# Kernel tuning notes

Hardware: AMD Instinct MI355X
Metric: run time of the kernel (lower is better)

## Reference

```python
import jax, jax.numpy as jnp
import numpy as np

CODEBOOK_SIZE = 1024
LATENT_DIM = 64
BETA = 0.25

def setup_inputs() -> dict:
    key = jax.random.key(0)
    k1, k2 = jax.random.split(key)
    B, C, T = 32, LATENT_DIM, 4096
    x = jax.random.normal(k1, (B, C, T), dtype=jnp.float32)
    # codebook initialized uniform(-1/K, 1/K) as in the torch module
    emb = jax.random.uniform(k2, (CODEBOOK_SIZE, LATENT_DIM), dtype=jnp.float32,
                             minval=-1.0 / CODEBOOK_SIZE, maxval=1.0 / CODEBOOK_SIZE)
    return {"x": x, "emb": emb}

def reference(x, emb):
    B, C, T = x.shape  # C == LATENT_DIM
    xf = jnp.transpose(x, (0, 2, 1)).reshape(B * T, C)  # [BT, D]
    d = (jnp.sum(xf * xf, axis=-1, keepdims=True)
         + jnp.sum(emb * emb, axis=-1)[None, :]
         - 2.0 * jnp.matmul(xf, emb.T))  # [BT, K]
    idx = jnp.argmin(d, axis=-1)  # [BT] int
    q = emb[idx].reshape(B, T, C).transpose(0, 2, 1)  # [B, C, T]
    commitment_loss = BETA * jnp.mean((jax.lax.stop_gradient(q) - x) ** 2)
    codebook_loss = jnp.mean((q - jax.lax.stop_gradient(x)) ** 2)
    quant_out = x + jax.lax.stop_gradient(q - x)  # straight-through
    return quant_out, codebook_loss, commitment_loss, idx.reshape(B, T)
```

## Files before the change

### kernel.cpp

```cpp
#include <hip/hip_runtime.h>


typedef unsigned long long u64;
typedef unsigned short u16;
typedef __attribute__((ext_vector_type(8))) short bf8_t;
typedef __attribute__((ext_vector_type(4))) float f4_t;

#define KCB 1024
#define DD 64
#define BB 32
#define TT 4096
#define BT (BB * TT)
#define NELEM (BB * DD * TT)

#define RPB 128
#define NT 16
#define FB_MAX 48
#define BAND 4e-5f

#define WS_LOSS 0
#define WS_E2 64
#define WS_EH 2048
#define WS_EL 34816

static __device__ __forceinline__ u16 bf16rte(float f) {
    unsigned u = __float_as_uint(f);
    return (u16)((u + 0x7FFFu + ((u >> 16) & 1u)) >> 16);
}
static __device__ __forceinline__ unsigned flipf(float f) {
    unsigned u = __float_as_uint(f);
    return (u & 0x80000000u) ? ~u : (u | 0x80000000u);
}
static __device__ __forceinline__ int fragidx(int n, int d) {
    return 1024 * (n >> 4) + 512 * (d >> 5) + 128 * ((d >> 3) & 3)
         + 8 * (n & 15) + (d & 7);
}

__global__ void vq_prep(const float* __restrict__ emb, float* __restrict__ ws) {
#pragma clang fp contract(off)
    const int tid = threadIdx.x;
    const int kl = tid >> 6, d = tid & 63;
    const int k = blockIdx.x * 4 + kl;
    if (blockIdx.x == 0 && tid == 0) ws[WS_LOSS] = 0.0f;
    __shared__ float sq[4][64];
    __shared__ float rsh[4][8];
    float v = emb[(size_t)k * DD + d];
    u16 hb = bf16rte(v);
    float hv = __uint_as_float((unsigned)hb << 16);
    u16 lb = bf16rte(v - hv);
    u16* ehg = (u16*)(ws + WS_EH) + 4096 * (k >> 6);
    u16* elg = (u16*)(ws + WS_EL) + 4096 * (k >> 6);
    const int ia = fragidx(k & 63, d);
    ehg[ia] = hb; elg[ia] = lb;
    sq[kl][d] = v * v;
    __syncthreads();
    if (tid < 32) {
        const int g = tid >> 3, j = tid & 7;
        float r = sq[g][j];
#pragma unroll
        for (int i = 1; i < 8; ++i) r += sq[g][8 * i + j];
        rsh[g][j] = r;
    }
    __syncthreads();
    if (tid < 4) {
        const float* r = rsh[tid];
        ws[WS_E2 + blockIdx.x * 4 + tid] =
            ((r[0] + r[1]) + (r[2] + r[3])) + ((r[4] + r[5]) + (r[6] + r[7]));
    }
}

__launch_bounds__(256, 4)
__global__ void vq_main(const float* __restrict__ x, const float* __restrict__ emb,
                        float* __restrict__ out, float* __restrict__ ws) {
#pragma clang fp contract(off)
    const int tid = threadIdx.x;
    const int lane = tid & 63;
    const int w = __builtin_amdgcn_readfirstlane(tid >> 6);
    const int l15 = lane & 15, q = lane >> 4;

    const int row0 = blockIdx.x * RPB;
    const int b = row0 >> 12;
    const int t0 = row0 & (TT - 1);

    __shared__ __align__(16) char arena[32768];
    u16* xhT = (u16*)arena;
    u16* xlT = (u16*)(arena + 16384);
    float* efs = (float*)arena;
    float* xfb = (float*)(arena + 16640);

    __shared__ float e2l[KCB];
    __shared__ float Srow[RPB];
    __shared__ int kwin[RPB];
    __shared__ int fbrows[FB_MAX];
    __shared__ int fbcnt;
    __shared__ float bsum;

    if (tid == 0) { fbcnt = 0; bsum = 0.0f; }
#pragma unroll
    for (int i = tid; i < KCB; i += 256) e2l[i] = ws[WS_E2 + i];

    if (tid < RPB) {
        const int r = tid;
        const float* xr = x + (size_t)b * DD * TT + t0 + r;
        const int gb = 1024 * (r >> 4);
        float rr[8];
#pragma unroll
        for (int i = 0; i < 64; i += 8) {
#pragma unroll
            for (int j = 0; j < 8; ++j) {
                float v = xr[(size_t)(i + j) * TT];
                if (i == 0) rr[j] = v * v; else rr[j] += v * v;
                u16 hb = bf16rte(v);
                float hv = __uint_as_float((unsigned)hb << 16);
                u16 lb = bf16rte(v - hv);
                const int ia = gb + fragidx(r & 15, i + j);
                xhT[ia] = hb; xlT[ia] = lb;
            }
        }
        Srow[r] = ((rr[0] + rr[1]) + (rr[2] + rr[3])) + ((rr[4] + rr[5]) + (rr[6] + rr[7]));
    }
    __syncthreads();

    bf8_t ah[2][2], al[2][2];
#pragma unroll
    for (int g = 0; g < 2; ++g) {
        const int gg = 2 * w + g;
        ah[g][0] = *(const bf8_t*)&xhT[1024 * gg + 8 * lane];
        ah[g][1] = *(const bf8_t*)&xhT[1024 * gg + 512 + 8 * lane];
        al[g][0] = *(const bf8_t*)&xlT[1024 * gg + 8 * lane];
        al[g][1] = *(const bf8_t*)&xlT[1024 * gg + 512 + 8 * lane];
    }
    float Sv[8];
#pragma unroll
    for (int g = 0; g < 2; ++g)
#pragma unroll
        for (int rg = 0; rg < 4; ++rg)
            Sv[4 * g + rg] = Srow[32 * w + 16 * g + 4 * q + rg];

    float v1[8], v2[8], kf[8];
#pragma unroll
    for (int s = 0; s < 8; ++s) { v1[s] = 3.4e38f; v2[s] = 3.4e38f; kf[s] = 0.0f; }

    const u16* ehg = (const u16*)(ws + WS_EH);
    const u16* elg = (const u16*)(ws + WS_EL);

    auto kstep = [&](float e2v, float kcol,
                     bf8_t bh0, bf8_t bl0, bf8_t bh1, bf8_t bl1) {
#pragma unroll
        for (int g = 0; g < 2; ++g) {
            f4_t acc = (f4_t){0.f, 0.f, 0.f, 0.f};
            acc = __builtin_amdgcn_mfma_f32_16x16x32_bf16(ah[g][0], bh0, acc, 0, 0, 0);
            acc = __builtin_amdgcn_mfma_f32_16x16x32_bf16(ah[g][0], bl0, acc, 0, 0, 0);
            acc = __builtin_amdgcn_mfma_f32_16x16x32_bf16(al[g][0], bh0, acc, 0, 0, 0);
            acc = __builtin_amdgcn_mfma_f32_16x16x32_bf16(ah[g][1], bh1, acc, 0, 0, 0);
            acc = __builtin_amdgcn_mfma_f32_16x16x32_bf16(ah[g][1], bl1, acc, 0, 0, 0);
            acc = __builtin_amdgcn_mfma_f32_16x16x32_bf16(al[g][1], bh1, acc, 0, 0, 0);
#pragma unroll
            for (int rg = 0; rg < 4; ++rg) {
                const int s = 4 * g + rg;
                float ck = Sv[s] + e2v;
                float u = __builtin_fmaf(-2.0f, acc[rg], ck);
                bool lt = u < v1[s];
                float sp = lt ? v1[s] : u;
                v2[s] = fminf(v2[s], sp);
                kf[s] = lt ? kcol : kf[s];
                v1[s] = fminf(v1[s], u);
            }
        }
    };

    bf8_t cbh0 = *(const bf8_t*)&ehg[8 * lane];
    bf8_t cbh1 = *(const bf8_t*)&ehg[512 + 8 * lane];
    bf8_t cbl0 = *(const bf8_t*)&elg[8 * lane];
    bf8_t cbl1 = *(const bf8_t*)&elg[512 + 8 * lane];
    float ce2 = e2l[l15];
#pragma unroll 2
    for (int it = 0; it < 63; ++it) {
        const u16* bhp = ehg + 1024 * (it + 1);
        const u16* blp = elg + 1024 * (it + 1);
        bf8_t nbh0 = *(const bf8_t*)&bhp[8 * lane];
        bf8_t nbh1 = *(const bf8_t*)&bhp[512 + 8 * lane];
        bf8_t nbl0 = *(const bf8_t*)&blp[8 * lane];
        bf8_t nbl1 = *(const bf8_t*)&blp[512 + 8 * lane];
        float ne2 = e2l[16 * (it + 1) + l15];
        kstep(ce2, (float)(16 * it + l15), cbh0, cbl0, cbh1, cbl1);
        cbh0 = nbh0; cbh1 = nbh1; cbl0 = nbl0; cbl1 = nbl1; ce2 = ne2;
    }
    kstep(ce2, (float)(16 * 63 + l15), cbh0, cbl0, cbh1, cbl1);

#pragma unroll
    for (int m = 1; m < 16; m <<= 1) {
#pragma unroll
        for (int s = 0; s < 8; ++s) {
            float ov1 = __shfl_xor(v1[s], m, 16);
            float okf = __shfl_xor(kf[s], m, 16);
            float ov2 = __shfl_xor(v2[s], m, 16);
            float nmx = fmaxf(v1[s], ov1);
            v2[s] = fminf(fminf(v2[s], ov2), nmx);
            bool lt = ov1 < v1[s];
            kf[s] = lt ? okf : kf[s];
            v1[s] = fminf(v1[s], ov1);
        }
    }
    if (l15 == 0) {
#pragma unroll
        for (int g = 0; g < 2; ++g)
#pragma unroll
            for (int rg = 0; rg < 4; ++rg) {
                const int s = 4 * g + rg;
                const int r = 32 * w + 16 * g + 4 * q + rg;
                kwin[r] = (int)kf[s];
                if (v2[s] <= v1[s] + BAND) {
                    int i = atomicAdd(&fbcnt, 1);
                    if (i < FB_MAX) fbrows[i] = r;
                }
            }
    }
    __syncthreads();

    const int cnt = min(fbcnt, FB_MAX);
    if (cnt > 0) {
        for (int i = tid; i < cnt * 64; i += 256) {
            int fi = i >> 6, l = i & 63;
            xfb[fi * 65 + l] = x[(size_t)b * DD * TT + (size_t)l * TT + t0 + fbrows[fi]];
        }
        u64 pmin[12];
#pragma unroll
        for (int sl = 0; sl < 12; ++sl) pmin[sl] = ~0ull;
#pragma unroll 1
        for (int T2 = 0; T2 < NT; ++T2) {
            __syncthreads();
            {
                const int n = tid >> 2, qd = (tid & 3) * 16;
                const float* sp = emb + (size_t)(T2 * 64 + n) * DD + qd;
                float* dp = efs + n * 65 + qd;
#pragma unroll
                for (int j = 0; j < 16; ++j) dp[j] = sp[j];
            }
            __syncthreads();
#pragma unroll
            for (int sl = 0; sl < 12; ++sl) {
                const int fi = w + 4 * sl;
                if (fi < cnt) {
                    float acc = 0.0f;
#pragma unroll
                    for (int i = 0; i < 64; ++i)
                        acc = __builtin_fmaf(efs[lane * 65 + i], xfb[fi * 65 + i], acc);
                    float ck = Srow[fbrows[fi]] + e2l[T2 * 64 + lane];
                    float u = __builtin_fmaf(-2.0f, acc, ck);
                    u64 pk = ((u64)flipf(u) << 10) | (unsigned)(T2 * 64 + lane);
                    pmin[sl] = pmin[sl] < pk ? pmin[sl] : pk;
                }
            }
        }
#pragma unroll
        for (int sl = 0; sl < 12; ++sl) {
            const int fi = w + 4 * sl;
            if (fi < cnt) {
                u64 pk = pmin[sl];
#pragma unroll
                for (int dl = 32; dl > 0; dl >>= 1) {
                    u64 o = __shfl_xor(pk, dl);
                    pk = o < pk ? o : pk;
                }
                if (lane == 0) kwin[fbrows[fi]] = (int)(pk & 1023u);
            }
        }
        __syncthreads();
    }

    if (tid < RPB) out[NELEM + 2 + row0 + tid] = (float)kwin[tid];

    const int r = tid & 127, c0 = (tid >> 7) * 32;
    const int kw = kwin[r];
    const float* eqr = emb + (size_t)kw * DD;
    float lsum = 0.0f;
#pragma unroll 8
    for (int i = 0; i < 32; ++i) {
        const int c = c0 + i;
        const size_t o = (size_t)b * DD * TT + (size_t)c * TT + t0 + r;
        float qv = eqr[c];
        float xv = x[o];
        out[o] = qv;
        float a = qv - xv;
        lsum = __builtin_fmaf(a, a, lsum);
    }
#pragma unroll
    for (int off = 32; off > 0; off >>= 1) lsum += __shfl_down(lsum, off);
    if (lane == 0) atomicAdd(&bsum, lsum);
    __syncthreads();
    if (tid == 0) atomicAdd(ws + WS_LOSS, bsum);
}

__global__ void vq_finalize(const float* __restrict__ ws, float* __restrict__ out) {
    if (threadIdx.x == 0 && blockIdx.x == 0) {
        float M = ws[WS_LOSS] / (float)NELEM;
        out[NELEM + 0] = M;
        out[NELEM + 1] = 0.25f * M;
    }
}

extern "C" void kernel_launch(void* const* d_in, const int* in_sizes, int n_in,
                              void* d_out, int out_size, void* d_ws, size_t ws_size,
                              hipStream_t stream) {
    const float* x = (const float*)d_in[0];
    const float* emb = (const float*)d_in[1];
    float* out = (float*)d_out;
    float* ws = (float*)d_ws;

    vq_prep<<<KCB / 4, 256, 0, stream>>>(emb, ws);
    vq_main<<<BT / RPB, 256, 0, stream>>>(x, emb, out, ws);
    vq_finalize<<<1, 64, 0, stream>>>(ws, out);
}
```

Measured before the change: 192.0 us.

## Split x staging across all threads, simplify fallback rescoring, fuse finalize via last-block counter

The x load and bf16 hi/lo split now uses all 256 threads, each doing half the channels, with partial squared norms combined through shared memory. The fallback exact-distance pass no longer stages codebook tiles and x rows in LDS behind per-tile barriers. Each warp instead handles its rows independently, reading emb from global and broadcasting x with shuffles. The separate finalize kernel is removed: the last block, found with an atomic counter, writes the loss, which saves a launch but adds fences and an atomic per block.

```diff
diff --git a/kernel.cpp b/kernel.cpp
--- a/kernel.cpp
+++ b/kernel.cpp
@@ -16,9 +16,11 @@
 #define RPB 128
 #define NT 16
 #define FB_MAX 48
+#define NSL 12
 #define BAND 4e-5f
 
 #define WS_LOSS 0
+#define WS_CNT 1
 #define WS_E2 64
 #define WS_EH 2048
 #define WS_EL 34816
@@ -41,7 +43,10 @@
     const int tid = threadIdx.x;
     const int kl = tid >> 6, d = tid & 63;
     const int k = blockIdx.x * 4 + kl;
-    if (blockIdx.x == 0 && tid == 0) ws[WS_LOSS] = 0.0f;
+    if (blockIdx.x == 0 && tid == 0) {
+        ws[WS_LOSS] = 0.0f;
+        ((unsigned*)ws)[WS_CNT] = 0u;
+    }
     __shared__ float sq[4][64];
     __shared__ float rsh[4][8];
     float v = emb[(size_t)k * DD + d];
@@ -85,11 +90,10 @@
     __shared__ __align__(16) char arena[32768];
     u16* xhT = (u16*)arena;
     u16* xlT = (u16*)(arena + 16384);
-    float* efs = (float*)arena;
-    float* xfb = (float*)(arena + 16640);
 
     __shared__ float e2l[KCB];
     __shared__ float Srow[RPB];
+    __shared__ float pbuf[RPB];
     __shared__ int kwin[RPB];
     __shared__ int fbrows[FB_MAX];
     __shared__ int fbcnt;
@@ -99,27 +103,31 @@
 #pragma unroll
     for (int i = tid; i < KCB; i += 256) e2l[i] = ws[WS_E2 + i];
 
-    if (tid < RPB) {
-        const int r = tid;
-        const float* xr = x + (size_t)b * DD * TT + t0 + r;
-        const int gb = 1024 * (r >> 4);
-        float rr[8];
+    const int r_ = tid & 127, h_ = tid >> 7;
+    float pp;
+    {
+        const float* xr = x + (size_t)b * DD * TT + t0 + r_;
+        const int gb = 1024 * (r_ >> 4);
+        float rr[4];
 #pragma unroll
         for (int i = 0; i < 64; i += 8) {
 #pragma unroll
-            for (int j = 0; j < 8; ++j) {
+            for (int jj = 0; jj < 4; ++jj) {
+                const int j = 4 * h_ + jj;
                 float v = xr[(size_t)(i + j) * TT];
-                if (i == 0) rr[j] = v * v; else rr[j] += v * v;
+                if (i == 0) rr[jj] = v * v; else rr[jj] += v * v;
                 u16 hb = bf16rte(v);
                 float hv = __uint_as_float((unsigned)hb << 16);
                 u16 lb = bf16rte(v - hv);
-                const int ia = gb + fragidx(r & 15, i + j);
+                const int ia = gb + fragidx(r_ & 15, i + j);
                 xhT[ia] = hb; xlT[ia] = lb;
             }
         }
-        Srow[r] = ((rr[0] + rr[1]) + (rr[2] + rr[3])) + ((rr[4] + rr[5]) + (rr[6] + rr[7]));
-    }
-    __syncthreads();
+        pp = (rr[0] + rr[1]) + (rr[2] + rr[3]);
+        if (h_ == 0) pbuf[r_] = pp;
+    }
+    __syncthreads();
+    if (h_ == 1) Srow[r_] = pbuf[r_] + pp;
 
     bf8_t ah[2][2], al[2][2];
 #pragma unroll
@@ -130,6 +138,7 @@
         al[g][0] = *(const bf8_t*)&xlT[1024 * gg + 8 * lane];
         al[g][1] = *(const bf8_t*)&xlT[1024 * gg + 512 + 8 * lane];
     }
+    __syncthreads();
     float Sv[8];
 #pragma unroll
     for (int g = 0; g < 2; ++g)
@@ -220,50 +229,32 @@
 
     const int cnt = min(fbcnt, FB_MAX);
     if (cnt > 0) {
-        for (int i = tid; i < cnt * 64; i += 256) {
-            int fi = i >> 6, l = i & 63;
-            xfb[fi * 65 + l] = x[(size_t)b * DD * TT + (size_t)l * TT + t0 + fbrows[fi]];
-        }
-        u64 pmin[12];
-#pragma unroll
-        for (int sl = 0; sl < 12; ++sl) pmin[sl] = ~0ull;
 #pragma unroll 1
-        for (int T2 = 0; T2 < NT; ++T2) {
-            __syncthreads();
-            {
-                const int n = tid >> 2, qd = (tid & 3) * 16;
-                const float* sp = emb + (size_t)(T2 * 64 + n) * DD + qd;
-                float* dp = efs + n * 65 + qd;
-#pragma unroll
-                for (int j = 0; j < 16; ++j) dp[j] = sp[j];
-            }
-            __syncthreads();
-#pragma unroll
-            for (int sl = 0; sl < 12; ++sl) {
-                const int fi = w + 4 * sl;
-                if (fi < cnt) {
+        for (int sl = 0; sl < NSL; ++sl) {
+            const int fi = w + 4 * sl;
+            if (fi < cnt) {
+                const int fr = fbrows[fi];
+                const float xv = x[(size_t)b * DD * TT + (size_t)lane * TT + t0 + fr];
+                const float srw = Srow[fr];
+                u64 pmin = ~0ull;
+#pragma unroll 1
+                for (int T2 = 0; T2 < NT; ++T2) {
+                    const float* er = emb + (size_t)(T2 * 64 + lane) * DD;
                     float acc = 0.0f;
 #pragma unroll
                     for (int i = 0; i < 64; ++i)
-                        acc = __builtin_fmaf(efs[lane * 65 + i], xfb[fi * 65 + i], acc);
-                    float ck = Srow[fbrows[fi]] + e2l[T2 * 64 + lane];
+                        acc = __builtin_fmaf(er[i], __shfl(xv, i), acc);
+                    float ck = srw + e2l[T2 * 64 + lane];
                     float u = __builtin_fmaf(-2.0f, acc, ck);
                     u64 pk = ((u64)flipf(u) << 10) | (unsigned)(T2 * 64 + lane);
-                    pmin[sl] = pmin[sl] < pk ? pmin[sl] : pk;
+                    pmin = pmin < pk ? pmin : pk;
                 }
-            }
-        }
-#pragma unroll
-        for (int sl = 0; sl < 12; ++sl) {
-            const int fi = w + 4 * sl;
-            if (fi < cnt) {
-                u64 pk = pmin[sl];
 #pragma unroll
                 for (int dl = 32; dl > 0; dl >>= 1) {
-                    u64 o = __shfl_xor(pk, dl);
-                    pk = o < pk ? o : pk;
+                    u64 o = __shfl_xor(pmin, dl);
+                    pmin = o < pmin ? o : pmin;
                 }
-                if (lane == 0) kwin[fbrows[fi]] = (int)(pk & 1023u);
+                if (lane == 0) kwin[fr] = (int)(pmin & 1023u);
             }
         }
         __syncthreads();
@@ -289,14 +280,17 @@
     for (int off = 32; off > 0; off >>= 1) lsum += __shfl_down(lsum, off);
     if (lane == 0) atomicAdd(&bsum, lsum);
     __syncthreads();
-    if (tid == 0) atomicAdd(ws + WS_LOSS, bsum);
-}
-
-__global__ void vq_finalize(const float* __restrict__ ws, float* __restrict__ out) {
-    if (threadIdx.x == 0 && blockIdx.x == 0) {
-        float M = ws[WS_LOSS] / (float)NELEM;
-        out[NELEM + 0] = M;
-        out[NELEM + 1] = 0.25f * M;
+
+    if (tid == 0) {
+        atomicAdd(ws + WS_LOSS, bsum);
+        __threadfence();
+        unsigned done = atomicAdd(&((unsigned*)ws)[WS_CNT], 1u);
+        if (done == (unsigned)(gridDim.x - 1)) {
+            __threadfence();
+            float M = atomicAdd(ws + WS_LOSS, 0.0f) / (float)NELEM;
+            out[NELEM + 0] = M;
+            out[NELEM + 1] = 0.25f * M;
+        }
     }
 }
 
@@ -310,5 +304,4 @@
 
     vq_prep<<<KCB / 4, 256, 0, stream>>>(emb, ws);
     vq_main<<<BT / RPB, 256, 0, stream>>>(x, emb, out, ws);
-    vq_finalize<<<1, 64, 0, stream>>>(ws, out);
-}
+}
```

New measurement: 280.9 us. 46.3% more time.

## Split codebook scan across two wave halves with 512-thread blocks and LDS merge

Applied to the files above, without the earlier changes.

Doubles the block to 512 threads. The two groups of four waves each scan half of the codebook for the same 128 rows, then merge their top-2 distances and argmins through shared memory before the fallback check. The fallback and output loops are rebalanced for the larger thread count. The aim is more waves in flight to hide MFMA and global-load latency, at the cost of extra barriers, a merge step, and possible occupancy limits from register pressure under launch_bounds(512,4).

```diff
diff --git a/kernel.cpp b/kernel.cpp
--- a/kernel.cpp
+++ b/kernel.cpp
@@ -14,8 +14,10 @@
 #define NELEM (BB * DD * TT)
 
 #define RPB 128
+#define NTHR 512
 #define NT 16
 #define FB_MAX 48
+#define NSL 6
 #define BAND 4e-5f
 
 #define WS_LOSS 0
@@ -69,13 +71,15 @@
     }
 }
 
-__launch_bounds__(256, 4)
+__launch_bounds__(NTHR, 4)
 __global__ void vq_main(const float* __restrict__ x, const float* __restrict__ emb,
                         float* __restrict__ out, float* __restrict__ ws) {
 #pragma clang fp contract(off)
     const int tid = threadIdx.x;
     const int lane = tid & 63;
     const int w = __builtin_amdgcn_readfirstlane(tid >> 6);
+    const int w4 = w & 3;
+    const int h = w >> 2;
     const int l15 = lane & 15, q = lane >> 4;
 
     const int row0 = blockIdx.x * RPB;
@@ -85,6 +89,9 @@
     __shared__ __align__(16) char arena[32768];
     u16* xhT = (u16*)arena;
     u16* xlT = (u16*)(arena + 16384);
+    float* mv1 = (float*)arena;
+    float* mv2 = (float*)(arena + 512);
+    float* mkf = (float*)(arena + 1024);
     float* efs = (float*)arena;
     float* xfb = (float*)(arena + 16640);
 
@@ -97,7 +104,7 @@
 
     if (tid == 0) { fbcnt = 0; bsum = 0.0f; }
 #pragma unroll
-    for (int i = tid; i < KCB; i += 256) e2l[i] = ws[WS_E2 + i];
+    for (int i = tid; i < KCB; i += NTHR) e2l[i] = ws[WS_E2 + i];
 
     if (tid < RPB) {
         const int r = tid;
@@ -124,7 +131,7 @@
     bf8_t ah[2][2], al[2][2];
 #pragma unroll
     for (int g = 0; g < 2; ++g) {
-        const int gg = 2 * w + g;
+        const int gg = 2 * w4 + g;
         ah[g][0] = *(const bf8_t*)&xhT[1024 * gg + 8 * lane];
         ah[g][1] = *(const bf8_t*)&xhT[1024 * gg + 512 + 8 * lane];
         al[g][0] = *(const bf8_t*)&xlT[1024 * gg + 8 * lane];
@@ -135,7 +142,8 @@
     for (int g = 0; g < 2; ++g)
 #pragma unroll
         for (int rg = 0; rg < 4; ++rg)
-            Sv[4 * g + rg] = Srow[32 * w + 16 * g + 4 * q + rg];
+            Sv[4 * g + rg] = Srow[32 * w4 + 16 * g + 4 * q + rg];
+    __syncthreads();
 
     float v1[8], v2[8], kf[8];
 #pragma unroll
@@ -169,13 +177,15 @@
         }
     };
 
-    bf8_t cbh0 = *(const bf8_t*)&ehg[8 * lane];
-    bf8_t cbh1 = *(const bf8_t*)&ehg[512 + 8 * lane];
-    bf8_t cbl0 = *(const bf8_t*)&elg[8 * lane];
-    bf8_t cbl1 = *(const bf8_t*)&elg[512 + 8 * lane];
-    float ce2 = e2l[l15];
+    const int it0 = 32 * h;
+    bf8_t cbh0 = *(const bf8_t*)&ehg[1024 * it0 + 8 * lane];
+    bf8_t cbh1 = *(const bf8_t*)&ehg[1024 * it0 + 512 + 8 * lane];
+    bf8_t cbl0 = *(const bf8_t*)&elg[1024 * it0 + 8 * lane];
+    bf8_t cbl1 = *(const bf8_t*)&elg[1024 * it0 + 512 + 8 * lane];
+    float ce2 = e2l[16 * it0 + l15];
 #pragma unroll 2
-    for (int it = 0; it < 63; ++it) {
+    for (int io = 0; io < 31; ++io) {
+        const int it = it0 + io;
         const u16* bhp = ehg + 1024 * (it + 1);
         const u16* blp = elg + 1024 * (it + 1);
         bf8_t nbh0 = *(const bf8_t*)&bhp[8 * lane];
@@ -186,7 +196,7 @@
         kstep(ce2, (float)(16 * it + l15), cbh0, cbl0, cbh1, cbl1);
         cbh0 = nbh0; cbh1 = nbh1; cbl0 = nbl0; cbl1 = nbl1; ce2 = ne2;
     }
-    kstep(ce2, (float)(16 * 63 + l15), cbh0, cbl0, cbh1, cbl1);
+    kstep(ce2, (float)(16 * (it0 + 31) + l15), cbh0, cbl0, cbh1, cbl1);
 
 #pragma unroll
     for (int m = 1; m < 16; m <<= 1) {
@@ -202,15 +212,33 @@
             v1[s] = fminf(v1[s], ov1);
         }
     }
-    if (l15 == 0) {
+
+    if (h == 1 && l15 == 0) {
 #pragma unroll
         for (int g = 0; g < 2; ++g)
 #pragma unroll
             for (int rg = 0; rg < 4; ++rg) {
                 const int s = 4 * g + rg;
-                const int r = 32 * w + 16 * g + 4 * q + rg;
-                kwin[r] = (int)kf[s];
-                if (v2[s] <= v1[s] + BAND) {
+                const int r = 32 * w4 + 16 * g + 4 * q + rg;
+                mv1[r] = v1[s]; mv2[r] = v2[s]; mkf[r] = kf[s];
+            }
+    }
+    __syncthreads();
+    if (h == 0 && l15 == 0) {
+#pragma unroll
+        for (int g = 0; g < 2; ++g)
+#pragma unroll
+            for (int rg = 0; rg < 4; ++rg) {
+                const int s = 4 * g + rg;
+                const int r = 32 * w4 + 16 * g + 4 * q + rg;
+                float v1b = mv1[r], v2b = mv2[r], kfb = mkf[r];
+                float nmx = fmaxf(v1[s], v1b);
+                float v2m = fminf(fminf(v2[s], v2b), nmx);
+                bool ltb = v1b < v1[s];
+                float kfm = ltb ? kfb : kf[s];
+                float v1m = fminf(v1[s], v1b);
+                kwin[r] = (int)kfm;
+                if (v2m <= v1m + BAND) {
                     int i = atomicAdd(&fbcnt, 1);
                     if (i < FB_MAX) fbrows[i] = r;
                 }
@@ -220,27 +248,27 @@
 
     const int cnt = min(fbcnt, FB_MAX);
     if (cnt > 0) {
-        for (int i = tid; i < cnt * 64; i += 256) {
+        for (int i = tid; i < cnt * 64; i += NTHR) {
             int fi = i >> 6, l = i & 63;
             xfb[fi * 65 + l] = x[(size_t)b * DD * TT + (size_t)l * TT + t0 + fbrows[fi]];
         }
-        u64 pmin[12];
-#pragma unroll
-        for (int sl = 0; sl < 12; ++sl) pmin[sl] = ~0ull;
+        u64 pmin[NSL];
+#pragma unroll
+        for (int sl = 0; sl < NSL; ++sl) pmin[sl] = ~0ull;
 #pragma unroll 1
         for (int T2 = 0; T2 < NT; ++T2) {
             __syncthreads();
             {
-                const int n = tid >> 2, qd = (tid & 3) * 16;
+                const int n = tid >> 3, qd = (tid & 7) * 8;
                 const float* sp = emb + (size_t)(T2 * 64 + n) * DD + qd;
                 float* dp = efs + n * 65 + qd;
 #pragma unroll
-                for (int j = 0; j < 16; ++j) dp[j] = sp[j];
+                for (int j = 0; j < 8; ++j) dp[j] = sp[j];
             }
             __syncthreads();
 #pragma unroll
-            for (int sl = 0; sl < 12; ++sl) {
-                const int fi = w + 4 * sl;
+            for (int sl = 0; sl < NSL; ++sl) {
+                const int fi = w + 8 * sl;
                 if (fi < cnt) {
                     float acc = 0.0f;
 #pragma unroll
@@ -254,8 +282,8 @@
             }
         }
 #pragma unroll
-        for (int sl = 0; sl < 12; ++sl) {
-            const int fi = w + 4 * sl;
+        for (int sl = 0; sl < NSL; ++sl) {
+            const int fi = w + 8 * sl;
             if (fi < cnt) {
                 u64 pk = pmin[sl];
 #pragma unroll
@@ -271,12 +299,12 @@
 
     if (tid < RPB) out[NELEM + 2 + row0 + tid] = (float)kwin[tid];
 
-    const int r = tid & 127, c0 = (tid >> 7) * 32;
+    const int r = tid & 127, c0 = (tid >> 7) * 16;
     const int kw = kwin[r];
     const float* eqr = emb + (size_t)kw * DD;
     float lsum = 0.0f;
 #pragma unroll 8
-    for (int i = 0; i < 32; ++i) {
+    for (int i = 0; i < 16; ++i) {
         const int c = c0 + i;
         const size_t o = (size_t)b * DD * TT + (size_t)c * TT + t0 + r;
         float qv = eqr[c];
@@ -309,6 +337,6 @@
     float* ws = (float*)d_ws;
 
     vq_prep<<<KCB / 4, 256, 0, stream>>>(emb, ws);
-    vq_main<<<BT / RPB, 256, 0, stream>>>(x, emb, out, ws);
+    vq_main<<<BT / RPB, NTHR, 0, stream>>>(x, emb, out, ws);
     vq_finalize<<<1, 64, 0, stream>>>(ws, out);
 }
```

After: 187.8 us, median of 2. 2.2% less time.
